# Performance work log

Hardware: AMD Instinct MI355X
Metric: run time of the kernel (lower is better)

The kernel has to match this reference:

```python
import jax, jax.numpy as jnp
import numpy as np

NUM_USERS = 100_000
NUM_ITEMS = 50_000
EMBED_DIM = 128
NUM_LAYERS = 3
NUM_PAIRS = 1_000_000  # user-item interactions; symmetrized -> 2M directed edges


def setup_inputs() -> dict:
    key = jax.random.key(0)
    k_u, k_i, k_eu, k_ei = jax.random.split(key, 4)
    N = NUM_USERS + NUM_ITEMS
    # Xavier-uniform init for embedding tables
    bound = float(np.sqrt(6.0 / (NUM_USERS + EMBED_DIM)))
    user_emb_w = jax.random.uniform(k_u, (NUM_USERS, EMBED_DIM), jnp.float32, -bound, bound)
    bound_i = float(np.sqrt(6.0 / (NUM_ITEMS + EMBED_DIM)))
    item_emb_w = jax.random.uniform(k_i, (NUM_ITEMS, EMBED_DIM), jnp.float32, -bound_i, bound_i)
    # bipartite interactions: user u <-> item (NUM_USERS + j); symmetrize directions
    users = jax.random.randint(k_eu, (NUM_PAIRS,), 0, NUM_USERS)
    items = jax.random.randint(k_ei, (NUM_PAIRS,), NUM_USERS, N)
    row = jnp.concatenate([users, items])
    col = jnp.concatenate([items, users])
    edge_index = jnp.stack([row, col]).astype(jnp.int64)  # [2, 2M]
    return {"edge_index": edge_index, "user_emb_w": user_emb_w, "item_emb_w": item_emb_w}


def _lightgcn_conv(x, row, col, num_nodes):
    # deg over target indices (col), as in pyg degree(col, N)
    deg = jax.ops.segment_sum(jnp.ones_like(col, dtype=x.dtype), col, num_segments=num_nodes)
    dinv = jnp.where(deg > 0, jax.lax.rsqrt(jnp.maximum(deg, 1.0)), 0.0)
    norm = dinv[row] * dinv[col]                      # [E]
    msg = norm[:, None] * x[row]                      # [E, D] gather + scale
    return jax.ops.segment_sum(msg, col, num_segments=num_nodes)  # scatter-add


def reference(edge_index, user_emb_w, item_emb_w):
    num_users = user_emb_w.shape[0]
    x = jnp.concatenate([user_emb_w, item_emb_w], axis=0)  # [N, D]
    N = x.shape[0]
    row, col = edge_index[0], edge_index[1]
    acc = x
    for _ in range(NUM_LAYERS):
        x = _lightgcn_conv(x, row, col, N)
        acc = acc + x
    final = acc / (NUM_LAYERS + 1)
    return final[:num_users], final[num_users:]
```

## Files before the change

### kernel.cpp

```cpp
#include <hip/hip_runtime.h>

#define NU 100000
#define NI 50000
#define NN 150000
#define DIM 128
#define NE 2000000
#define NP 1000000
#define NB ((NN + 63) / 64)
#define NSH 128
#define QSPLIT 4
#define QB ((NB + QSPLIT - 1) / QSPLIT)
#define CAP 32
#define BCAP 4096

typedef _Float16 half8 __attribute__((ext_vector_type(8)));
typedef _Float16 half4c __attribute__((ext_vector_type(4)));

#define PPS ((NP + NSH - 1) / NSH)
#define CVB ((NN * DIM / 4 + 255) / 256)

__global__ __launch_bounds__(256) void scatter_kernel(
    const int* __restrict__ row, const int* __restrict__ col,
    int* __restrict__ cfil, int* __restrict__ pairs) {
    __shared__ int lcnt[QB];
    int s = blockIdx.x & (NSH - 1);
    int q = blockIdx.x >> 7;
    int t = threadIdx.x;
    for (int i = t; i < QB; i += 256) lcnt[i] = 0;
    __syncthreads();
    int base = s * PPS;
    int lim = min(NP - base, PPS);
    int* pb = pairs + (size_t)s * NB * CAP;
    for (int i = t; i < lim; i += 256) {
        int k = base + i;
        int u = row[k];
        int v = col[k];
        int c1 = v >> 6;
        if ((c1 & 3) == q) {
            int p1 = atomicAdd(&lcnt[c1 >> 2], 1);
            if (p1 < CAP) pb[c1 * CAP + p1] = (u << 6) | (v & 63);
        }
        int c2 = u >> 6;
        if ((c2 & 3) == q) {
            int p2 = atomicAdd(&lcnt[c2 >> 2], 1);
            if (p2 < CAP) pb[c2 * CAP + p2] = (v << 6) | (u & 63);
        }
    }
    __syncthreads();
    for (int i = t; i < QB; i += 256) {
        int b = (i << 2) | q;
        if (b < NB) cfil[b * NSH + s] = min(lcnt[i], CAP);
    }
}

__global__ __launch_bounds__(256) void place_kernel(
    const int* __restrict__ cfil, const int* __restrict__ pairs,
    int* __restrict__ adj, int* __restrict__ ptr, int* __restrict__ deg,
    float* __restrict__ dinv,
    const float* __restrict__ user, const float* __restrict__ item,
    _Float16* __restrict__ x16) {
    __shared__ int lp[NSH * CAP];
    __shared__ int llen[NSH];
    __shared__ int lcnt[64];
    __shared__ int lptr[64];
    __shared__ int lfill[64];
    int blk = blockIdx.x;
    int t = threadIdx.x;
    if (blk < NB) {
        int b = blk;
        if (t < NSH) llen[t] = cfil[b * NSH + t];
        if (t < 64) { lcnt[t] = 0; lfill[t] = 0; }
        __syncthreads();
        #pragma unroll
        for (int slot = t; slot < NSH * CAP; slot += 256) {
            int s = slot >> 5;
            int i = slot & 31;
            lp[slot] = pairs[((size_t)s * NB + b) * CAP + i];
        }
        __syncthreads();
        #pragma unroll
        for (int slot = t; slot < NSH * CAP; slot += 256) {
            if ((slot & 31) < llen[slot >> 5])
                atomicAdd(&lcnt[lp[slot] & 63], 1);
        }
        __syncthreads();
        if (t < 64) {
            int v = lcnt[t];
            int incl = v;
            #pragma unroll
            for (int off = 1; off < 64; off <<= 1) {
                int u = __shfl_up(incl, off, 64);
                if (t >= off) incl += u;
            }
            lptr[t] = (b << 12) + incl - v;
            int c = (b << 6) + t;
            if (c < NN) {
                ptr[c] = lptr[t];
                deg[c] = v;
                dinv[c] = (v > 0) ? 1.0f / sqrtf((float)v) : 0.0f;
            }
        }
        __syncthreads();
        #pragma unroll
        for (int slot = t; slot < NSH * CAP; slot += 256) {
            if ((slot & 31) < llen[slot >> 5]) {
                int pk = lp[slot];
                int lc = pk & 63;
                int so = lptr[lc] + atomicAdd(&lfill[lc], 1);
                adj[so] = pk >> 6;
            }
        }
    } else {
        size_t tt = (size_t)(blk - NB) * 256 + t;
        size_t e = tt * 4;
        if (e < (size_t)NN * DIM) {
            const size_t NUsz = (size_t)NU * DIM;
            float4 v = (e < NUsz) ? *(const float4*)(user + e)
                                  : *(const float4*)(item + (e - NUsz));
            half4c h;
            h[0] = (_Float16)v.x; h[1] = (_Float16)v.y;
            h[2] = (_Float16)v.z; h[3] = (_Float16)v.w;
            *(half4c*)(x16 + e) = h;
        }
    }
}

__global__ __launch_bounds__(256) void prop_kernel(
    const _Float16* __restrict__ xin,
    const float* __restrict__ dinv, const int* __restrict__ ptr,
    const int* __restrict__ deg, const int* __restrict__ adj,
    _Float16* __restrict__ xout, int finalize,
    const _Float16* __restrict__ x0, const _Float16* __restrict__ x1,
    const _Float16* __restrict__ x2, float* __restrict__ out)
{
    int wid = (blockIdx.x * blockDim.x + threadIdx.x) >> 6;
    if (wid >= NN) return;
    int lane = threadIdx.x & 63;
    int q = lane >> 4;
    int m = lane & 15;
    int beg = ptr[wid];
    int end = beg + deg[wid];

    float a0 = 0.f, a1 = 0.f, a2 = 0.f, a3 = 0.f;
    float a4 = 0.f, a5 = 0.f, a6 = 0.f, a7 = 0.f;
    int j = beg;
    for (; j + 8 <= end; j += 8) {
        int r0 = adj[j + q];
        int r1 = adj[j + 4 + q];
        float w0 = dinv[r0];
        float w1 = dinv[r1];
        half8 v0 = *(const half8*)(xin + (size_t)r0 * DIM + 8 * m);
        half8 v1 = *(const half8*)(xin + (size_t)r1 * DIM + 8 * m);
        a0 += w0 * (float)v0[0] + w1 * (float)v1[0];
        a1 += w0 * (float)v0[1] + w1 * (float)v1[1];
        a2 += w0 * (float)v0[2] + w1 * (float)v1[2];
        a3 += w0 * (float)v0[3] + w1 * (float)v1[3];
        a4 += w0 * (float)v0[4] + w1 * (float)v1[4];
        a5 += w0 * (float)v0[5] + w1 * (float)v1[5];
        a6 += w0 * (float)v0[6] + w1 * (float)v1[6];
        a7 += w0 * (float)v0[7] + w1 * (float)v1[7];
    }
    if (j < end) {
        int jj0 = j + q;
        int jj1 = j + 4 + q;
        int r0 = adj[min(jj0, end - 1)];
        int r1 = adj[min(jj1, end - 1)];
        float w0 = (jj0 < end) ? dinv[r0] : 0.f;
        float w1 = (jj1 < end) ? dinv[r1] : 0.f;
        half8 v0 = *(const half8*)(xin + (size_t)r0 * DIM + 8 * m);
        half8 v1 = *(const half8*)(xin + (size_t)r1 * DIM + 8 * m);
        a0 += w0 * (float)v0[0] + w1 * (float)v1[0];
        a1 += w0 * (float)v0[1] + w1 * (float)v1[1];
        a2 += w0 * (float)v0[2] + w1 * (float)v1[2];
        a3 += w0 * (float)v0[3] + w1 * (float)v1[3];
        a4 += w0 * (float)v0[4] + w1 * (float)v1[4];
        a5 += w0 * (float)v0[5] + w1 * (float)v1[5];
        a6 += w0 * (float)v0[6] + w1 * (float)v1[6];
        a7 += w0 * (float)v0[7] + w1 * (float)v1[7];
    }
    a0 += __shfl_xor(a0, 16, 64); a1 += __shfl_xor(a1, 16, 64);
    a2 += __shfl_xor(a2, 16, 64); a3 += __shfl_xor(a3, 16, 64);
    a4 += __shfl_xor(a4, 16, 64); a5 += __shfl_xor(a5, 16, 64);
    a6 += __shfl_xor(a6, 16, 64); a7 += __shfl_xor(a7, 16, 64);
    a0 += __shfl_xor(a0, 32, 64); a1 += __shfl_xor(a1, 32, 64);
    a2 += __shfl_xor(a2, 32, 64); a3 += __shfl_xor(a3, 32, 64);
    a4 += __shfl_xor(a4, 32, 64); a5 += __shfl_xor(a5, 32, 64);
    a6 += __shfl_xor(a6, 32, 64); a7 += __shfl_xor(a7, 32, 64);

    if (q != 0) return;
    float dc = dinv[wid];
    float n0 = dc * a0, n1 = dc * a1, n2 = dc * a2, n3 = dc * a3;
    float n4 = dc * a4, n5 = dc * a5, n6 = dc * a6, n7 = dc * a7;

    if (!finalize) {
        half8 h;
        h[0] = (_Float16)n0; h[1] = (_Float16)n1; h[2] = (_Float16)n2; h[3] = (_Float16)n3;
        h[4] = (_Float16)n4; h[5] = (_Float16)n5; h[6] = (_Float16)n6; h[7] = (_Float16)n7;
        *(half8*)(xout + (size_t)wid * DIM + 8 * m) = h;
    } else {
        size_t base = (size_t)wid * DIM + 8 * m;
        half8 f0 = *(const half8*)(x0 + base);
        half8 f1 = *(const half8*)(x1 + base);
        half8 f2 = *(const half8*)(x2 + base);
        float* po = out + base;
        float4 oa, ob;
        oa.x = ((float)f0[0] + (float)f1[0] + (float)f2[0] + n0) * 0.25f;
        oa.y = ((float)f0[1] + (float)f1[1] + (float)f2[1] + n1) * 0.25f;
        oa.z = ((float)f0[2] + (float)f1[2] + (float)f2[2] + n2) * 0.25f;
        oa.w = ((float)f0[3] + (float)f1[3] + (float)f2[3] + n3) * 0.25f;
        ob.x = ((float)f0[4] + (float)f1[4] + (float)f2[4] + n4) * 0.25f;
        ob.y = ((float)f0[5] + (float)f1[5] + (float)f2[5] + n5) * 0.25f;
        ob.z = ((float)f0[6] + (float)f1[6] + (float)f2[6] + n6) * 0.25f;
        ob.w = ((float)f0[7] + (float)f1[7] + (float)f2[7] + n7) * 0.25f;
        *(float4*)(po) = oa;
        *(float4*)(po + 4) = ob;
    }
}


extern "C" void kernel_launch(void* const* d_in, const int* in_sizes, int n_in,
                              void* d_out, int out_size, void* d_ws, size_t ws_size,
                              hipStream_t stream) {
    const int* edge = (const int*)d_in[0];
    const int* row = edge;
    const int* col = edge + NE;
    const float* user = (const float*)d_in[1];
    const float* item = (const float*)d_in[2];
    float* out = (float*)d_out;

    char* ws = (char*)d_ws;
    size_t off = 0;
    auto alloc = [&](size_t bytes) -> void* {
        void* p = ws + off;
        off = (off + bytes + 255) & ~(size_t)255;
        return p;
    };
    _Float16* x0 = (_Float16*)alloc(sizeof(_Float16) * (size_t)NN * DIM);
    _Float16* x1 = (_Float16*)alloc(sizeof(_Float16) * (size_t)NN * DIM);
    _Float16* x2 = (_Float16*)alloc(sizeof(_Float16) * (size_t)NN * DIM);
    float* dinv = (float*)alloc(sizeof(float) * NN);
    int*   cfil = (int*)  alloc(sizeof(int) * NSH * NB);
    int*   ptr  = (int*)  alloc(sizeof(int) * NN);
    int*   deg  = (int*)  alloc(sizeof(int) * NN);
    int*   pairs= (int*)  alloc(sizeof(int) * (size_t)NSH * NB * CAP);
    int*   adj  = (int*)  alloc(sizeof(int) * (size_t)NB * BCAP);

    scatter_kernel<<<NSH * QSPLIT, 256, 0, stream>>>(row, col, cfil, pairs);
    place_kernel<<<NB + CVB, 256, 0, stream>>>(cfil, pairs, adj, ptr, deg, dinv,
                                               user, item, x0);

    int blocks = (NN + 3) / 4;
    prop_kernel<<<blocks, 256, 0, stream>>>(x0, dinv, ptr, deg, adj, x1, 0,
                                            nullptr, nullptr, nullptr, nullptr);
    prop_kernel<<<blocks, 256, 0, stream>>>(x1, dinv, ptr, deg, adj, x2, 0,
                                            nullptr, nullptr, nullptr, nullptr);
    prop_kernel<<<blocks, 256, 0, stream>>>(x2, dinv, ptr, deg, adj, nullptr, 1,
                                            x0, x1, x2, out);
}
```

Baseline: 454.1 us.

## Split fp16 conversion across scatter and place kernels, widen scatter split

The fp32-to-fp16 conversion of the embedding table is divided in half. The first half now runs as extra blocks in the scatter kernel and the second half stays in the place kernel, so each conversion half overlaps with the graph-building work. The scatter kernel's bucket split rises from 4 to 8, giving more blocks with fewer shared counters each, and the place kernel now loads pairs with int4 vectors. These extra blocks and the higher QSPLIT launch more blocks, and each scatter block reads the full edge stream and discards more edges.

```diff
diff --git a/kernel.cpp b/kernel.cpp
--- a/kernel.cpp
+++ b/kernel.cpp
@@ -4,12 +4,12 @@
 #define NI 50000
 #define NN 150000
 #define DIM 128
-#define NE 2000000
 #define NP 1000000
 #define NB ((NN + 63) / 64)
 #define NSH 128
-#define QSPLIT 4
+#define QSPLIT 8
 #define QB ((NB + QSPLIT - 1) / QSPLIT)
+#define NSCT (NSH * QSPLIT)
 #define CAP 32
 #define BCAP 4096
 
@@ -17,39 +17,62 @@
 typedef _Float16 half4c __attribute__((ext_vector_type(4)));
 
 #define PPS ((NP + NSH - 1) / NSH)
-#define CVB ((NN * DIM / 4 + 255) / 256)
+#define CVH 9375
+#define HALFE 9600000
+
+__device__ __forceinline__ void convert_block(
+    size_t e0, int t, const float* __restrict__ user,
+    const float* __restrict__ item, _Float16* __restrict__ x16) {
+    size_t e = e0 + (size_t)t * 4;
+    if (e < (size_t)NN * DIM) {
+        const size_t NUsz = (size_t)NU * DIM;
+        float4 v = (e < NUsz) ? *(const float4*)(user + e)
+                              : *(const float4*)(item + (e - NUsz));
+        half4c h;
+        h[0] = (_Float16)v.x; h[1] = (_Float16)v.y;
+        h[2] = (_Float16)v.z; h[3] = (_Float16)v.w;
+        *(half4c*)(x16 + e) = h;
+    }
+}
 
 __global__ __launch_bounds__(256) void scatter_kernel(
     const int* __restrict__ row, const int* __restrict__ col,
-    int* __restrict__ cfil, int* __restrict__ pairs) {
-    __shared__ int lcnt[QB];
-    int s = blockIdx.x & (NSH - 1);
-    int q = blockIdx.x >> 7;
+    int* __restrict__ cfil, int* __restrict__ pairs,
+    const float* __restrict__ user, const float* __restrict__ item,
+    _Float16* __restrict__ x16) {
+    int blk = blockIdx.x;
     int t = threadIdx.x;
-    for (int i = t; i < QB; i += 256) lcnt[i] = 0;
-    __syncthreads();
-    int base = s * PPS;
-    int lim = min(NP - base, PPS);
-    int* pb = pairs + (size_t)s * NB * CAP;
-    for (int i = t; i < lim; i += 256) {
-        int k = base + i;
-        int u = row[k];
-        int v = col[k];
-        int c1 = v >> 6;
-        if ((c1 & 3) == q) {
-            int p1 = atomicAdd(&lcnt[c1 >> 2], 1);
-            if (p1 < CAP) pb[c1 * CAP + p1] = (u << 6) | (v & 63);
-        }
-        int c2 = u >> 6;
-        if ((c2 & 3) == q) {
-            int p2 = atomicAdd(&lcnt[c2 >> 2], 1);
-            if (p2 < CAP) pb[c2 * CAP + p2] = (v << 6) | (u & 63);
-        }
-    }
-    __syncthreads();
-    for (int i = t; i < QB; i += 256) {
-        int b = (i << 2) | q;
-        if (b < NB) cfil[b * NSH + s] = min(lcnt[i], CAP);
+    if (blk < NSCT) {
+        __shared__ int lcnt[QB];
+        int s = blk & (NSH - 1);
+        int q = blk >> 7;
+        for (int i = t; i < QB; i += 256) lcnt[i] = 0;
+        __syncthreads();
+        int base = s * PPS;
+        int lim = min(NP - base, PPS);
+        int* pb = pairs + (size_t)s * NB * CAP;
+        for (int i = t; i < lim; i += 256) {
+            int k = base + i;
+            int u = row[k];
+            int v = col[k];
+            int c1 = v >> 6;
+            if ((c1 & 7) == q) {
+                int p1 = atomicAdd(&lcnt[c1 >> 3], 1);
+                if (p1 < CAP) pb[c1 * CAP + p1] = (u << 6) | (v & 63);
+            }
+            int c2 = u >> 6;
+            if ((c2 & 7) == q) {
+                int p2 = atomicAdd(&lcnt[c2 >> 3], 1);
+                if (p2 < CAP) pb[c2 * CAP + p2] = (v << 6) | (u & 63);
+            }
+        }
+        __syncthreads();
+        for (int i = t; i < QB; i += 256) {
+            int b = (i << 3) | q;
+            if (b < NB) cfil[b * NSH + s] = min(lcnt[i], CAP);
+        }
+    } else {
+        convert_block((size_t)(blk - NSCT) * 1024, t, user, item, x16);
     }
 }
 
@@ -71,11 +94,13 @@
         if (t < NSH) llen[t] = cfil[b * NSH + t];
         if (t < 64) { lcnt[t] = 0; lfill[t] = 0; }
         __syncthreads();
+        int4* lp4 = (int4*)lp;
         #pragma unroll
-        for (int slot = t; slot < NSH * CAP; slot += 256) {
-            int s = slot >> 5;
-            int i = slot & 31;
-            lp[slot] = pairs[((size_t)s * NB + b) * CAP + i];
+        for (int p = 0; p < 4; p++) {
+            int idx = p * 256 + t;
+            int ci = idx >> 3;
+            int j = idx & 7;
+            lp4[idx] = ((const int4*)pairs)[(((size_t)ci * NB + b) << 3) + j];
         }
         __syncthreads();
         #pragma unroll
@@ -111,17 +136,7 @@
             }
         }
     } else {
-        size_t tt = (size_t)(blk - NB) * 256 + t;
-        size_t e = tt * 4;
-        if (e < (size_t)NN * DIM) {
-            const size_t NUsz = (size_t)NU * DIM;
-            float4 v = (e < NUsz) ? *(const float4*)(user + e)
-                                  : *(const float4*)(item + (e - NUsz));
-            half4c h;
-            h[0] = (_Float16)v.x; h[1] = (_Float16)v.y;
-            h[2] = (_Float16)v.z; h[3] = (_Float16)v.w;
-            *(half4c*)(x16 + e) = h;
-        }
+        convert_block((size_t)HALFE + (size_t)(blk - NB) * 1024, t, user, item, x16);
     }
 }
 
@@ -223,7 +238,7 @@
                               hipStream_t stream) {
     const int* edge = (const int*)d_in[0];
     const int* row = edge;
-    const int* col = edge + NE;
+    const int* col = edge + 2 * NP;
     const float* user = (const float*)d_in[1];
     const float* item = (const float*)d_in[2];
     float* out = (float*)d_out;
@@ -245,8 +260,9 @@
     int*   pairs= (int*)  alloc(sizeof(int) * (size_t)NSH * NB * CAP);
     int*   adj  = (int*)  alloc(sizeof(int) * (size_t)NB * BCAP);
 
-    scatter_kernel<<<NSH * QSPLIT, 256, 0, stream>>>(row, col, cfil, pairs);
-    place_kernel<<<NB + CVB, 256, 0, stream>>>(cfil, pairs, adj, ptr, deg, dinv,
+    scatter_kernel<<<NSCT + CVH, 256, 0, stream>>>(row, col, cfil, pairs,
+                                                   user, item, x0);
+    place_kernel<<<NB + CVH, 256, 0, stream>>>(cfil, pairs, adj, ptr, deg, dinv,
                                                user, item, x0);
 
     int blocks = (NN + 3) / 4;
```

New measurement: 453.0 us. About the same (-0.3%).
